# Kernel tuning notes

Measured on AMD Instinct MI355X. Metric: run time of the kernel, lower is better.

Reference implementation:

```python
import math
import jax, jax.numpy as jnp
import numpy as np

D_MODEL = 512
N_HEADS = 8
HEAD_DIM = D_MODEL // N_HEADS
B, T = 2, 2048


def _sinusoid_pe(T, d):
    # Transformer-XL relative sinusoids for distances -(T-1)..(T-1) -> (2T-1, d)
    pos = jnp.arange(-(T - 1), T, dtype=jnp.float32)
    div = jnp.exp(2.0 * jnp.arange(d // 2, dtype=jnp.float32) * (-math.log(10000.0) / d))
    terms = pos[:, None] * div[None, :]
    pe = jnp.zeros((2 * T - 1, d), dtype=jnp.float32)
    pe = pe.at[:, 0::2].set(jnp.sin(terms)).at[:, 1::2].set(jnp.cos(terms))
    return pe


def _relative_shift(s):
    # s: (B, H, T, 2T-1) -> shifted (B, H, T, T)
    b, h, t, l = s.shape
    s = jnp.pad(s, ((0, 0), (0, 0), (0, 0), (1, 0)))        # (B,H,T,2T)
    s = s.reshape(b, h, l + 1, t)[:, :, 1:, :].reshape(b, h, t, l)
    return s[:, :, :, :t]


def setup_inputs() -> dict:
    key = jax.random.key(0)
    ks = jax.random.split(key, 12)
    sw = 1.0 / math.sqrt(D_MODEL)
    su = math.sqrt(6.0 / (N_HEADS + HEAD_DIM))  # xavier_uniform bound
    inp = {
        "x": jax.random.normal(ks[0], (B, T, D_MODEL), jnp.float32),
        "mask": jnp.ones((B, 1, T, T), jnp.int32),
        "Wq": jax.random.normal(ks[1], (D_MODEL, D_MODEL), jnp.float32) * sw,
        "bq": jax.random.normal(ks[2], (D_MODEL,), jnp.float32) * 0.01,
        "Wv": jax.random.normal(ks[3], (D_MODEL, D_MODEL), jnp.float32) * sw,
        "bv": jax.random.normal(ks[4], (D_MODEL,), jnp.float32) * 0.01,
        "Wkc": jax.random.normal(ks[5], (D_MODEL, D_MODEL), jnp.float32) * sw,
        "bkc": jax.random.normal(ks[6], (D_MODEL,), jnp.float32) * 0.01,
        "Wkl": jax.random.normal(ks[7], (D_MODEL, D_MODEL), jnp.float32) * sw,
        "bkl": jax.random.normal(ks[8], (D_MODEL,), jnp.float32) * 0.01,
        "u": jax.random.uniform(ks[9], (N_HEADS, HEAD_DIM), jnp.float32, -su, su),
        "v": jax.random.uniform(ks[10], (N_HEADS, HEAD_DIM), jnp.float32, -su, su),
    }
    return inp


def reference(x, mask, Wq, bq, Wv, bv, Wkc, bkc, Wkl, bkl, u, v):
    b, t, d = x.shape
    h, hd = u.shape
    pe = _sinusoid_pe(t, d)                                   # (2T-1, D)
    q = (x @ Wq.T + bq).reshape(b, t, h, hd)                  # (B,T,H,hd)
    val = (x @ Wv.T + bv).reshape(b, t, h, hd)                # (B,T,H,hd)
    kc = (x @ Wkc.T + bkc).reshape(b, t, h, hd)               # (B,T,H,hd)
    kl = (pe @ Wkl.T + bkl).reshape(2 * t - 1, h, hd)         # (2T-1,H,hd)
    ac = jnp.einsum('bqhd,bkhd->bhqk', q + u, kc)             # content score
    bd = jnp.einsum('bqhd,lhd->bhql', q + v, kl)              # position score
    bd = _relative_shift(bd)                                  # (B,H,T,T)
    attn = (ac + bd) / math.sqrt(hd)
    attn = jnp.where(mask == 0, -jnp.inf, attn)
    p = jax.nn.softmax(attn, axis=-1)
    out = jnp.einsum('bhqk,bkhd->bqhd', p, val)
    return out.reshape(b, t, d)
```

## Files before the change

### kernel.cpp

```cpp
#include <hip/hip_runtime.h>
#include <hip/hip_bf16.h>

#define BB 2
#define TT 2048
#define DD 512
#define HH 8
#define HD 64

typedef __bf16 bf16;
typedef __bf16 bf16x8 __attribute__((ext_vector_type(8)));
typedef float f32x4 __attribute__((ext_vector_type(4)));
typedef unsigned int u32;

#define SCL 0.1803368801111204f

static __device__ __forceinline__ f32x4 mfma16(bf16x8 a, bf16x8 b, f32x4 c) {
  return __builtin_amdgcn_mfma_f32_16x16x32_bf16(a, b, c, 0, 0, 0);
}
static __device__ __forceinline__ u32 cvtpk(float lo, float hi) {
  u32 r; asm("v_cvt_pk_bf16_f32 %0, %1, %2" : "=v"(r) : "v"(lo), "v"(hi)); return r;
}
#define PERM(a, b, s) __builtin_amdgcn_perm((a), (b), (s))

#define GL16(gp, lp) __builtin_amdgcn_global_load_lds( \
    (const __attribute__((address_space(1))) unsigned int*)(gp), \
    (__attribute__((address_space(3))) unsigned int*)(lp), 16, 0, 0)

__global__ __launch_bounds__(256) void prep_kernel(
    const float* __restrict__ x,
    const float* __restrict__ Wq, const float* __restrict__ Wkc,
    const float* __restrict__ Wv, const float* __restrict__ Wkl,
    bf16* __restrict__ xb, bf16* __restrict__ wqb, bf16* __restrict__ wkcb,
    bf16* __restrict__ wvb, bf16* __restrict__ wklb, bf16* __restrict__ peb)
{
  int bid = blockIdx.x;
  int tid = threadIdx.x;
  if (bid < 1536) {
    const float* src; bf16* dst; int off;
    if (bid < 1024) { src = x; dst = xb; off = bid * 2048 + tid * 8; }
    else {
      int g = (bid - 1024) >> 7;
      src = (g == 0) ? Wq : (g == 1) ? Wkc : (g == 2) ? Wv : Wkl;
      dst = (g == 0) ? wqb : (g == 1) ? wkcb : (g == 2) ? wvb : wklb;
      off = ((bid - 1024) & 127) * 2048 + tid * 8;
    }
    float4 v0 = *(const float4*)(src + off);
    float4 v1 = *(const float4*)(src + off + 4);
    bf16 o[8] = {(bf16)v0.x,(bf16)v0.y,(bf16)v0.z,(bf16)v0.w,
                 (bf16)v1.x,(bf16)v1.y,(bf16)v1.z,(bf16)v1.w};
    *(bf16x8*)(dst + off) = *(bf16x8*)o;
  } else {
    int p = (bid - 1536) * 2048 + tid * 8;
    int row = p >> 8;
    int pc = p & 255;
    float pos = (float)(row - (TT - 1));
    bool valid = (row < 2 * TT - 1);
#pragma unroll
    for (int j = 0; j < 8; ++j) {
      int i = pc + j;
      float sv = 0.f, cv = 0.f;
      if (valid) {
        float div = exp2f((float)i * -0.051905124764638574f);
        float t = pos * div;
        sv = __sinf(t); cv = __cosf(t);
      }
      peb[(size_t)row * DD + 2 * i]     = (bf16)sv;
      peb[(size_t)row * DD + 2 * i + 1] = (bf16)cv;
    }
  }
}

__global__ __launch_bounds__(256) void gemm_all(
    const bf16* __restrict__ xb, const bf16* __restrict__ peb,
    const bf16* __restrict__ wq, const bf16* __restrict__ wkc,
    const bf16* __restrict__ wv, const bf16* __restrict__ wkl,
    const float* __restrict__ bq, const float* __restrict__ bkc,
    const float* __restrict__ bv, const float* __restrict__ bkl,
    const float* __restrict__ uu, const float* __restrict__ vv,
    bf16* __restrict__ qu, bf16* __restrict__ qv, bf16* __restrict__ kc,
    bf16* __restrict__ vt, bf16* __restrict__ kl)
{
  __shared__ __align__(16) bf16 Al[2][128 * 64];
  __shared__ __align__(16) bf16 Bl[2][128 * 64];

  int bid = blockIdx.x;
  int j = bid >> 3;
  int n_tile = ((bid & 7) << 1) | (j >> 5);
  int m_tile = j & 31;
  int mode = n_tile >> 2;
  int n0 = (n_tile & 3) * 128;
  int m0 = m_tile * 128;

  int tid = threadIdx.x;
  int w = tid >> 6, lane = tid & 63;
  int lr = lane & 15, lg = lane >> 4;
  int wr = w >> 1, wc = w & 1;

  const bf16* A = (mode == 3) ? peb : xb;
  const bf16* W = (mode == 0) ? wq : (mode == 1) ? wkc : (mode == 2) ? wv : wkl;
  const float* bias = (mode == 0) ? bq : (mode == 1) ? bkc : (mode == 2) ? bv : bkl;

  int srow = w * 32 + (lane >> 3);
  int schunk = (lane & 7) ^ (lane >> 3);
  const bf16* Abase = A + (size_t)(m0 + srow) * DD + 8 * schunk;
  const bf16* Wbase = W + (size_t)(n0 + srow) * DD + 8 * schunk;

  auto STAGE = [&](int buf, int k0) {
#pragma unroll
    for (int i = 0; i < 4; ++i) {
      GL16(Abase + (size_t)i * 8 * DD + k0, &Al[buf][(w * 32 + i * 8) * 64]);
      GL16(Wbase + (size_t)i * 8 * DD + k0, &Bl[buf][(w * 32 + i * 8) * 64]);
    }
  };

  f32x4 acc[4][4];
#pragma unroll
  for (int tm = 0; tm < 4; ++tm)
#pragma unroll
    for (int tn = 0; tn < 4; ++tn) acc[tm][tn] = (f32x4){0.f, 0.f, 0.f, 0.f};

  STAGE(0, 0);
  __syncthreads();

#pragma unroll 1
  for (int kk = 0; kk < 8; ++kk) {
    int cur = kk & 1;
    if (kk < 7) STAGE(cur ^ 1, (kk + 1) * 64);
    const bf16* Ab = Al[cur];
    const bf16* Bb = Bl[cur];
#pragma unroll
    for (int s = 0; s < 2; ++s) {
      bf16x8 af[4], bfr[4];
#pragma unroll
      for (int t = 0; t < 4; ++t) {
        int arow = wr * 64 + 16 * t + lr;
        af[t]  = *(const bf16x8*)(Ab + arow * 64 + 8 * ((4 * s + lg) ^ (lr & 7)));
        int brow = wc * 64 + 16 * t + lr;
        bfr[t] = *(const bf16x8*)(Bb + brow * 64 + 8 * ((4 * s + lg) ^ (lr & 7)));
      }
#pragma unroll
      for (int tm = 0; tm < 4; ++tm)
#pragma unroll
        for (int tn = 0; tn < 4; ++tn)
          acc[tm][tn] = mfma16(af[tm], bfr[tn], acc[tm][tn]);
    }
    __syncthreads();
  }

#pragma unroll
  for (int tn = 0; tn < 4; ++tn) {
    int n = n0 + wc * 64 + 16 * tn + lr;
    float bn = bias[n];
    int h = n >> 6, d = n & 63;
    float ua = 0.f, va = 0.f;
    if (mode == 0) { ua = uu[h * HD + d]; va = vv[h * HD + d]; }
#pragma unroll
    for (int tm = 0; tm < 4; ++tm) {
#pragma unroll
      for (int r = 0; r < 4; ++r) {
        int m = m0 + wr * 64 + 16 * tm + lg * 4 + r;
        float val = acc[tm][tn][r] + bn;
        if (mode == 0) {
          int bb = m >> 11, tp = m & (TT - 1);
          size_t idx = ((size_t)(bb * HH + h) * TT + tp) * HD + d;
          qu[idx] = (bf16)((val + ua) * SCL);
          qv[idx] = (bf16)((val + va) * SCL);
        } else if (mode == 1) {
          int bb = m >> 11, tp = m & (TT - 1);
          kc[((size_t)(bb * HH + h) * TT + tp) * HD + d] = (bf16)val;
        } else if (mode == 2) {
          int bb = m >> 11, tp = m & (TT - 1);
          vt[((size_t)(bb * HH + h) * HD + d) * TT + tp] = (bf16)val;
        } else {
          kl[((size_t)h * 4096 + m) * HD + d] = (bf16)val;
        }
      }
    }
  }
}

__global__ __launch_bounds__(512) void attn_kernel(
    const bf16* __restrict__ QU, const bf16* __restrict__ QV,
    const bf16* __restrict__ KC, const bf16* __restrict__ VT,
    const bf16* __restrict__ KL, bf16* __restrict__ pacc, float* __restrict__ psum)
{
  __shared__ __align__(16) bf16 kcL[2][64 * 64];
  __shared__ __align__(16) bf16 vtL[2][64 * 64];
  __shared__ __align__(16) bf16 klL[3][64 * 64];
  __shared__ __align__(16) bf16 PlS[8][16][40];

  int bid = blockIdx.x;
  int xcd = bid & 7, j = bid >> 3;
  int g = (xcd << 1) | (j >> 5);
  int qt = j & 31;
  int b = g >> 3, h = g & 7;
  int q0 = qt * 64;

  int tid = threadIdx.x;
  int w = tid >> 6;
  int lane = tid & 63;
  int lr = lane & 15, lg = lane >> 4;
  int qg = w & 3, kh = w >> 2;
  int qw = q0 + qg * 16;

  int rsub = lane >> 3, chunk = lane & 7;
  int srow = w * 8 + rsub;
  int csrc = chunk ^ rsub;
  int ldst = w * 512;

  const bf16* qu_bh = QU + (size_t)(b * HH + h) * TT * HD;
  const bf16* qv_bh = QV + (size_t)(b * HH + h) * TT * HD;
  const bf16* kc_bh = KC + (size_t)(b * HH + h) * TT * HD;
  const bf16* vt_bh = VT + (size_t)(b * HH + h) * HD * TT;
  const bf16* kl_h  = KL + (size_t)h * 4096 * HD;

  bf16x8 quf[2], qvf[2];
#pragma unroll
  for (int s = 0; s < 2; ++s) {
    quf[s] = *(const bf16x8*)(qu_bh + (size_t)(qw + lr) * HD + 32 * s + 8 * lg);
    qvf[s] = *(const bf16x8*)(qv_bh + (size_t)(qw + lr) * HD + 32 * s + 8 * lg);
  }

  int B0 = 1984 - q0;

  GL16(kc_bh + (size_t)srow * 64 + csrc * 8, &kcL[0][ldst]);
  GL16(vt_bh + (size_t)srow * TT + csrc * 8, &vtL[0][ldst]);
  GL16(kl_h + (size_t)(B0 + srow) * 64 + csrc * 8, &klL[0][ldst]);
  GL16(kl_h + (size_t)(B0 + 64 + srow) * 64 + csrc * 8, &klL[1][ldst]);
  __syncthreads();

  bf16* kcCur = kcL[0]; bf16* kcNxt = kcL[1];
  bf16* vtCur = vtL[0]; bf16* vtNxt = vtL[1];
  bf16* klA = klL[0];  bf16* klB = klL[1];  bf16* klC = klL[2];

  f32x4 accO[4];
#pragma unroll
  for (int t = 0; t < 4; ++t) accO[t] = (f32x4){0.f, 0.f, 0.f, 0.f};
  float plsum[4] = {0.f, 0.f, 0.f, 0.f};
  int wrow0 = 48 + 32 * kh - 16 * qg;
  int pchb = lr & 7;

  u32 pat[4]; int srcl[4];
#pragma unroll
  for (int r = 0; r < 4; ++r) {
    int row = lg * 4 + r;
    pat[r]  = (lr <= row) ? 0x05040000u : 0x07060000u;
    srcl[r] = (lane & 48) | ((15 + lr - row) & 15);
  }

#pragma unroll 1
  for (int kt = 0; kt < 32; ++kt) {
    int k0 = kt * 64;

    if (kt < 31) {
      int k1 = k0 + 64;
      int grb = B0 + 64 * kt + 128;
      GL16(kc_bh + (size_t)(k1 + srow) * 64 + csrc * 8, &kcNxt[ldst]);
      GL16(vt_bh + (size_t)srow * TT + k1 + csrc * 8, &vtNxt[ldst]);
      GL16(kl_h + (size_t)(grb + srow) * 64 + csrc * 8, &klC[ldst]);
    }

    f32x4 S[2], a[3];
#pragma unroll
    for (int t = 0; t < 2; ++t) {
      f32x4 acc = (f32x4){0.f, 0.f, 0.f, 0.f};
      int row = 32 * kh + 16 * t + lr;
#pragma unroll
      for (int s = 0; s < 2; ++s) {
        int pch = (4 * s + lg) ^ pchb;
        bf16x8 kb = *(const bf16x8*)(&kcCur[row * 64 + pch * 8]);
        acc = mfma16(quf[s], kb, acc);
      }
      S[t] = acc;
    }

#pragma unroll
    for (int t = 0; t < 3; ++t) {
      f32x4 acc = (f32x4){0.f, 0.f, 0.f, 0.f};
      int row = wrow0 + 16 * t + lr;
      const bf16* kb_base = (row & 64) ? klB : klA;
      int off = row & 63;
#pragma unroll
      for (int s = 0; s < 2; ++s) {
        int pch = (4 * s + lg) ^ pchb;
        bf16x8 kb = *(const bf16x8*)(&kb_base[off * 64 + pch * 8]);
        acc = mfma16(qvf[s], kb, acc);
      }
      a[t] = acc;
    }

    float p[2][4];
#pragma unroll
    for (int t = 0; t < 2; ++t) {
#pragma unroll
      for (int r = 0; r < 4; ++r) {
        u32 pk = cvtpk(a[t][r], a[t + 1][r]);
        u32 gb = __shfl(pk, srcl[r], 64);
        float wv = __builtin_bit_cast(float, PERM(gb, 0u, pat[r]));
        float e = __builtin_exp2f(S[t][r] + wv);
        p[t][r] = e;
        plsum[r] += e;
      }
    }

#pragma unroll
    for (int r = 0; r < 4; ++r) {
      PlS[w][4 * lg + r][lr]      = (bf16)p[0][r];
      PlS[w][4 * lg + r][16 + lr] = (bf16)p[1][r];
    }
    {
      bf16x8 pa = *(const bf16x8*)(&PlS[w][lr][8 * lg]);
#pragma unroll
      for (int t = 0; t < 4; ++t) {
        int row = 16 * t + lr;
        int pch = (4 * kh + lg) ^ pchb;
        bf16x8 vb = *(const bf16x8*)(&vtCur[row * 64 + pch * 8]);
        accO[t] = mfma16(pa, vb, accO[t]);
      }
    }

    __syncthreads();

    bf16* tmp;
    tmp = kcCur; kcCur = kcNxt; kcNxt = tmp;
    tmp = vtCur; vtCur = vtNxt; vtNxt = tmp;
    tmp = klA; klA = klB; klB = klC; klC = tmp;
  }

#pragma unroll
  for (int msk = 1; msk < 16; msk <<= 1)
#pragma unroll
    for (int r = 0; r < 4; ++r) plsum[r] += __shfl_xor(plsum[r], msk, 64);

  int pid = (bid << 1) | kh;
#pragma unroll
  for (int r = 0; r < 4; ++r) {
    int qr = qg * 16 + 4 * lg + r;
#pragma unroll
    for (int t = 0; t < 4; ++t)
      pacc[(size_t)pid * 4096 + qr * 64 + 16 * t + lr] = (bf16)accO[t][r];
    if (lr == 0) psum[pid * 64 + qr] = plsum[r];
  }
}

__global__ __launch_bounds__(256) void reduce_kernel(
    const bf16* __restrict__ pacc, const float* __restrict__ psum,
    float* __restrict__ out)
{
  int pb = blockIdx.x;
  int xcd = pb & 7, j = pb >> 3;
  int g = (xcd << 1) | (j >> 5);
  int qt = j & 31;
  int b = g >> 3, h = g & 7;
  int bidA = pb * 2, bidB = pb * 2 + 1;

  int t = threadIdx.x;
  int qr = t >> 2, d0 = (t & 3) * 16;

  const bf16* pA = pacc + (size_t)bidA * 4096 + qr * 64 + d0;
  const bf16* pB = pacc + (size_t)bidB * 4096 + qr * 64 + d0;
  float inv = 1.f / (psum[bidA * 64 + qr] + psum[bidB * 64 + qr]);

  int q = qt * 64 + qr;
  float* op = out + (size_t)(b * TT + q) * DD + h * HD + d0;
  bf16x8 a0 = *(const bf16x8*)pA;
  bf16x8 a1 = *(const bf16x8*)(pA + 8);
  bf16x8 b0 = *(const bf16x8*)pB;
  bf16x8 b1 = *(const bf16x8*)(pB + 8);
#pragma unroll
  for (int i = 0; i < 8; ++i) {
    op[i]     = ((float)a0[i] + (float)b0[i]) * inv;
    op[i + 8] = ((float)a1[i] + (float)b1[i]) * inv;
  }
}

extern "C" void kernel_launch(void* const* d_in, const int* in_sizes, int n_in,
                              void* d_out, int out_size, void* d_ws, size_t ws_size,
                              hipStream_t stream) {
  const float* x   = (const float*)d_in[0];
  const float* Wq  = (const float*)d_in[2];
  const float* bq  = (const float*)d_in[3];
  const float* Wv  = (const float*)d_in[4];
  const float* bv  = (const float*)d_in[5];
  const float* Wkc = (const float*)d_in[6];
  const float* bkc = (const float*)d_in[7];
  const float* Wkl = (const float*)d_in[8];
  const float* bkl = (const float*)d_in[9];
  const float* u   = (const float*)d_in[10];
  const float* v   = (const float*)d_in[11];
  float* out = (float*)d_out;

  char* ws = (char*)d_ws;
  const size_t MB = 1024 * 1024;
  bf16* xb   = (bf16*)(ws + 0);
  bf16* peb  = (bf16*)(ws + 4 * MB);
  bf16* wqb  = (bf16*)(ws + 8 * MB);
  bf16* wkcb = (bf16*)(ws + 8 * MB + 512 * 1024);
  bf16* wvb  = (bf16*)(ws + 9 * MB);
  bf16* wklb = (bf16*)(ws + 9 * MB + 512 * 1024);
  bf16* qu   = (bf16*)(ws + 10 * MB);
  bf16* qv   = (bf16*)(ws + 14 * MB);
  bf16* kc   = (bf16*)(ws + 18 * MB);
  bf16* vt   = (bf16*)(ws + 22 * MB);
  bf16* kl   = (bf16*)(ws + 26 * MB);
  bf16* pacc = (bf16*)(ws + 30 * MB);
  float* psum = (float*)(ws + 38 * MB);

  prep_kernel<<<2048, 256, 0, stream>>>(x, Wq, Wkc, Wv, Wkl,
                                        xb, wqb, wkcb, wvb, wklb, peb);
  gemm_all<<<512, 256, 0, stream>>>(xb, peb, wqb, wkcb, wvb, wklb,
                                    bq, bkc, bv, bkl, u, v,
                                    qu, qv, kc, vt, kl);
  attn_kernel<<<512, 512, 0, stream>>>(qu, qv, kc, vt, kl, pacc, psum);
  reduce_kernel<<<512, 256, 0, stream>>>(pacc, psum, out);
}
```

Before: 101.1 us.

## Fuse split-K reduction into attention kernel via LDS and add MFMA priority hints

```diff
diff --git a/kernel.cpp b/kernel.cpp
--- a/kernel.cpp
+++ b/kernel.cpp
@@ -182,7 +182,7 @@
 __global__ __launch_bounds__(512) void attn_kernel(
     const bf16* __restrict__ QU, const bf16* __restrict__ QV,
     const bf16* __restrict__ KC, const bf16* __restrict__ VT,
-    const bf16* __restrict__ KL, bf16* __restrict__ pacc, float* __restrict__ psum)
+    const bf16* __restrict__ KL, float* __restrict__ out)
 {
   __shared__ __align__(16) bf16 kcL[2][64 * 64];
   __shared__ __align__(16) bf16 vtL[2][64 * 64];
@@ -261,6 +261,7 @@
     }
 
     f32x4 S[2], a[3];
+    __builtin_amdgcn_s_setprio(1);
 #pragma unroll
     for (int t = 0; t < 2; ++t) {
       f32x4 acc = (f32x4){0.f, 0.f, 0.f, 0.f};
@@ -288,6 +289,7 @@
       }
       a[t] = acc;
     }
+    __builtin_amdgcn_s_setprio(0);
 
     float p[2][4];
 #pragma unroll
@@ -310,6 +312,7 @@
     }
     {
       bf16x8 pa = *(const bf16x8*)(&PlS[w][lr][8 * lg]);
+      __builtin_amdgcn_s_setprio(1);
 #pragma unroll
       for (int t = 0; t < 4; ++t) {
         int row = 16 * t + lr;
@@ -317,6 +320,7 @@
         bf16x8 vb = *(const bf16x8*)(&vtCur[row * 64 + pch * 8]);
         accO[t] = mfma16(pa, vb, accO[t]);
       }
+      __builtin_amdgcn_s_setprio(0);
     }
 
     __syncthreads();
@@ -332,45 +336,29 @@
 #pragma unroll
     for (int r = 0; r < 4; ++r) plsum[r] += __shfl_xor(plsum[r], msk, 64);
 
-  int pid = (bid << 1) | kh;
-#pragma unroll
-  for (int r = 0; r < 4; ++r) {
-    int qr = qg * 16 + 4 * lg + r;
-#pragma unroll
-    for (int t = 0; t < 4; ++t)
-      pacc[(size_t)pid * 4096 + qr * 64 + 16 * t + lr] = (bf16)accO[t][r];
-    if (lr == 0) psum[pid * 64 + qr] = plsum[r];
-  }
-}
-
-__global__ __launch_bounds__(256) void reduce_kernel(
-    const bf16* __restrict__ pacc, const float* __restrict__ psum,
-    float* __restrict__ out)
-{
-  int pb = blockIdx.x;
-  int xcd = pb & 7, j = pb >> 3;
-  int g = (xcd << 1) | (j >> 5);
-  int qt = j & 31;
-  int b = g >> 3, h = g & 7;
-  int bidA = pb * 2, bidB = pb * 2 + 1;
-
-  int t = threadIdx.x;
-  int qr = t >> 2, d0 = (t & 3) * 16;
-
-  const bf16* pA = pacc + (size_t)bidA * 4096 + qr * 64 + d0;
-  const bf16* pB = pacc + (size_t)bidB * 4096 + qr * 64 + d0;
-  float inv = 1.f / (psum[bidA * 64 + qr] + psum[bidB * 64 + qr]);
-
-  int q = qt * 64 + qr;
-  float* op = out + (size_t)(b * TT + q) * DD + h * HD + d0;
-  bf16x8 a0 = *(const bf16x8*)pA;
-  bf16x8 a1 = *(const bf16x8*)(pA + 8);
-  bf16x8 b0 = *(const bf16x8*)pB;
-  bf16x8 b1 = *(const bf16x8*)(pB + 8);
-#pragma unroll
-  for (int i = 0; i < 8; ++i) {
-    op[i]     = ((float)a0[i] + (float)b0[i]) * inv;
-    op[i + 8] = ((float)a1[i] + (float)b1[i]) * inv;
+  float* rO = (float*)klL;
+  float* rS = (float*)PlS;
+  if (kh == 1) {
+#pragma unroll
+    for (int r = 0; r < 4; ++r) {
+      int qr = (qg * 16 + 4 * lg + r) * 68;
+#pragma unroll
+      for (int t = 0; t < 4; ++t) rO[qr + 16 * t + lr] = accO[t][r];
+      if (lr == 0) rS[qg * 16 + 4 * lg + r] = plsum[r];
+    }
+  }
+  __syncthreads();
+  if (kh == 0) {
+#pragma unroll
+    for (int r = 0; r < 4; ++r) {
+      int qloc = qg * 16 + 4 * lg + r;
+      float inv = 1.f / (plsum[r] + rS[qloc]);
+      int q = qw + lg * 4 + r;
+      float* op = out + (size_t)(b * TT + q) * DD + h * HD;
+#pragma unroll
+      for (int t = 0; t < 4; ++t)
+        op[16 * t + lr] = (accO[t][r] + rO[qloc * 68 + 16 * t + lr]) * inv;
+    }
   }
 }
 
@@ -403,14 +391,11 @@
   bf16* kc   = (bf16*)(ws + 18 * MB);
   bf16* vt   = (bf16*)(ws + 22 * MB);
   bf16* kl   = (bf16*)(ws + 26 * MB);
-  bf16* pacc = (bf16*)(ws + 30 * MB);
-  float* psum = (float*)(ws + 38 * MB);
 
   prep_kernel<<<2048, 256, 0, stream>>>(x, Wq, Wkc, Wv, Wkl,
                                         xb, wqb, wkcb, wvb, wklb, peb);
   gemm_all<<<512, 256, 0, stream>>>(xb, peb, wqb, wkcb, wvb, wklb,
                                     bq, bkc, bv, bkl, u, v,
                                     qu, qv, kc, vt, kl);
-  attn_kernel<<<512, 512, 0, stream>>>(qu, qv, kc, vt, kl, pacc, psum);
-  reduce_kernel<<<512, 256, 0, stream>>>(pacc, psum, out);
-}
+  attn_kernel<<<512, 512, 0, stream>>>(qu, qv, kc, vt, kl, out);
+}
```

After: 95.36 us. 5.7% less time.
